# Optimization experiments

Measured on AMD Instinct MI355X. Metric: run time of the kernel, lower is better.

Reference implementation:

```python
import jax, jax.numpy as jnp
import numpy as np

NEG = -1e10
LN_EPS = 1e-5


def _layernorm(x, g, b):
    m = x.mean(-1, keepdims=True)
    v = ((x - m) ** 2).mean(-1, keepdims=True)
    return (x - m) / jnp.sqrt(v + LN_EPS) * g + b


def setup_inputs() -> dict:
    key = jax.random.key(0)
    ks = jax.random.split(key, 12)
    B, N, C, H, E = 8, 2048, 64, 2, 65536
    p = lambda i, shape: (jax.random.normal(ks[i], shape, jnp.float32) * 0.02)
    return {
        "x": jax.random.normal(ks[0], (B, N, C), jnp.float32),
        "edge": jax.random.randint(ks[1], (2, E), 0, N),
        "num_heads": H,
        "wq_d": p(2, (C, C)), "wk_d": p(3, (C, C)), "wv_d": p(4, (C, C)), "bv_d": jnp.zeros((C,), jnp.float32),
        "wq_s": p(5, (C, C)), "wk_s": p(6, (C, C)), "wv_s": p(7, (C, C)), "bv_s": jnp.zeros((C,), jnp.float32),
        "ln1_g": jnp.ones((C,), jnp.float32), "ln1_b": jnp.zeros((C,), jnp.float32),
        "ln2_g": jnp.ones((C,), jnp.float32), "ln2_b": jnp.zeros((C,), jnp.float32),
        "w1": p(8, (C, 2 * C)), "b1": jnp.zeros((2 * C,), jnp.float32),
        "w2": p(9, (2 * C, C)), "b2": jnp.zeros((C,), jnp.float32),
    }


def reference(x, edge, num_heads,
              wq_d, wk_d, wv_d, bv_d,
              wq_s, wk_s, wv_s, bv_s,
              ln1_g, ln1_b, ln2_g, ln2_b,
              w1, b1, w2, b2):
    B, N, C = x.shape
    H = num_heads
    d = C // H
    scale = C ** (-0.5)  # original scales by x.shape[-1]**-0.5, not head dim

    # ---- DMHSA: dynamic mean-threshold masked attention ----
    q = (x @ wq_d).reshape(B, N, H, d).transpose(0, 2, 1, 3)  # [B,H,N,d]
    k = (x @ wk_d).reshape(B, N, H, d).transpose(0, 2, 1, 3)
    v = (x @ wv_d + bv_d).reshape(B, N, H, d).transpose(0, 2, 1, 3)
    scores = jnp.einsum('bhnd,bhmd->bhnm', q, k) * scale  # [B,H,N,N]
    dyn_mask = scores >= scores.mean(-1, keepdims=True)
    attn_d = jax.nn.softmax(jnp.where(dyn_mask, scores, NEG), axis=-1)
    dyn_out = jnp.einsum('bhnm,bhmd->bnhd', attn_d, v).reshape(B, N, C)

    # ---- SSA: static graph-edge masked attention (single head) ----
    qs = x @ wq_s
    ks_ = x @ wk_s
    vs = x @ wv_s + bv_s
    scores_s = jnp.einsum('bnc,bmc->bnm', qs, ks_) * scale  # [B,N,N]
    edge_mask = jnp.zeros((N, N), bool).at[edge[0], edge[1]].set(True)
    attn_s = jax.nn.softmax(jnp.where(edge_mask[None], scores_s, NEG), axis=-1)
    static_out = jnp.einsum('bnm,bmc->bnc', attn_s, vs)

    # ---- residual + LN + MLP (two linears, no activation) + LN ----
    residual = dyn_out + static_out + x
    h = _layernorm(residual, ln1_g, ln1_b)
    h = (h @ w1 + b1) @ w2 + b2
    out = _layernorm(h + residual, ln2_g, ln2_b)
    return (out, attn_d)
```

## Files before the change

### kernel.cpp

```cpp
#include <hip/hip_runtime.h>
#include <hip/hip_bf16.h>

#define TB 256

constexpr int B_ = 8, N_ = 2048, H_ = 2;
constexpr float SCALE = 0.125f;
constexpr float NEGV = -1e10f;
constexpr float LN_EPS = 1e-5f;
constexpr size_t SCH = (size_t)B_ * N_ * 64;

typedef __attribute__((ext_vector_type(8))) short bf16x8;
typedef __attribute__((ext_vector_type(4))) float f32x4;
typedef __attribute__((ext_vector_type(8))) unsigned short us8;
typedef __attribute__((ext_vector_type(4))) unsigned short us4;

#define MFMA16(A, B, C) __builtin_amdgcn_mfma_f32_16x16x32_bf16((A), (B), (C), 0, 0, 0)

__device__ __forceinline__ unsigned short f2b(float f) {
  __hip_bfloat16 h = __float2bfloat16(f);
  return *reinterpret_cast<unsigned short*>(&h);
}
__device__ __forceinline__ float b2f(unsigned short u) {
  union { unsigned int i; float f; } v; v.i = ((unsigned int)u) << 16; return v.f;
}
__device__ __forceinline__ int swz(int off) { return off ^ (((off >> 12) & 7) << 4); }

__device__ __forceinline__ float wave_reduce_sum(float v) {
#pragma unroll
  for (int off = 32; off >= 1; off >>= 1) v += __shfl_xor(v, off, 64);
  return v;
}
__device__ __forceinline__ float wave_reduce_max(float v) {
#pragma unroll
  for (int off = 32; off >= 1; off >>= 1) v = fmaxf(v, __shfl_xor(v, off, 64));
  return v;
}

__global__ __launch_bounds__(TB) void proj_kernel(
    const float* __restrict__ x,
    const float* __restrict__ wqd, const float* __restrict__ wkd,
    const float* __restrict__ wvd, const float* __restrict__ bvd,
    const float* __restrict__ wqs, const float* __restrict__ wks,
    const float* __restrict__ wvs, const float* __restrict__ bvs,
    float* __restrict__ vd, float* __restrict__ vsb,
    unsigned short* __restrict__ q16d, unsigned short* __restrict__ k16d,
    unsigned short* __restrict__ q16s, unsigned short* __restrict__ k16s) {
  const int t = threadIdx.x;
  const int row = blockIdx.x * 16 + (t >> 4);
  const int cg = t & 15;
  const int b = row >> 11, n = row & 2047;
  float xr[64];
  const float4* xp = reinterpret_cast<const float4*>(x + (size_t)row * 64);
#pragma unroll
  for (int i = 0; i < 16; ++i) {
    float4 v = xp[i];
    xr[4 * i] = v.x; xr[4 * i + 1] = v.y; xr[4 * i + 2] = v.z; xr[4 * i + 3] = v.w;
  }
  const float* W[6] = {wqd, wkd, wvd, wqs, wks, wvs};
#pragma unroll
  for (int m = 0; m < 6; ++m) {
    float4 acc = make_float4(0.f, 0.f, 0.f, 0.f);
    if (m == 2) acc = reinterpret_cast<const float4*>(bvd)[cg];
    if (m == 5) acc = reinterpret_cast<const float4*>(bvs)[cg];
    const float4* wp = reinterpret_cast<const float4*>(W[m]) + cg;
#pragma unroll
    for (int c = 0; c < 64; ++c) {
      float4 w4 = wp[(size_t)c * 16];
      float s = xr[c];
      acc.x += s * w4.x; acc.y += s * w4.y; acc.z += s * w4.z; acc.w += s * w4.w;
    }
    if (m == 2) {
      reinterpret_cast<float4*>(vd + (size_t)row * 64)[cg] = acc;
    } else if (m == 5) {
      reinterpret_cast<float4*>(vsb + (size_t)row * 64)[cg] = acc;
    } else {
      float sc = (m == 0 || m == 3) ? SCALE : 1.f;
      us4 o; o.x = f2b(acc.x * sc); o.y = f2b(acc.y * sc);
      o.z = f2b(acc.z * sc); o.w = f2b(acc.w * sc);
      if (m == 0 || m == 1) {
        unsigned short* dst = (m == 0) ? q16d : k16d;
        size_t idx = ((size_t)(b * 2 + (cg >> 3)) * 2048 + n) * 32 + (cg & 7) * 4;
        *reinterpret_cast<us4*>(dst + idx) = o;
      } else {
        unsigned short* dst = (m == 3) ? q16s : k16s;
        *reinterpret_cast<us4*>(dst + (size_t)row * 64 + cg * 4) = o;
      }
    }
  }
}

__global__ __launch_bounds__(TB) void tr32_kernel(const float* __restrict__ v,
                                                  unsigned short* __restrict__ vt) {
  __shared__ float tile[256][33];
  const int t = threadIdx.x;
  const int bh = blockIdx.y, b = bh >> 1, h = bh & 1;
  const int r0 = blockIdx.x * 256;
  const float* src = v + ((size_t)b * 2048 + r0) * 64 + h * 32;
#pragma unroll
  for (int i = 0; i < 8; ++i) {
    int f4 = t + i * 256;
    int row = f4 >> 3, c4 = f4 & 7;
    float4 xv = *reinterpret_cast<const float4*>(src + (size_t)row * 64 + c4 * 4);
    tile[row][c4 * 4 + 0] = xv.x; tile[row][c4 * 4 + 1] = xv.y;
    tile[row][c4 * 4 + 2] = xv.z; tile[row][c4 * 4 + 3] = xv.w;
  }
  __syncthreads();
  unsigned short* dstb = vt + (size_t)bh * 32 * 2048 + r0;
#pragma unroll
  for (int i = 0; i < 4; ++i) {
    int ch = t + i * 256;
    int d = ch >> 5, rb = ch & 31;
    us8 o;
#pragma unroll
    for (int e = 0; e < 8; ++e) o[e] = f2b(tile[rb * 8 + e][d]);
    *reinterpret_cast<us8*>(dstb + (size_t)d * 2048 + rb * 8) = o;
  }
}

__global__ __launch_bounds__(TB) void tr64_kernel(const float* __restrict__ v,
                                                  unsigned short* __restrict__ vt) {
  __shared__ float tile[128][65];
  const int t = threadIdx.x;
  const int b = blockIdx.y;
  const int r0 = blockIdx.x * 128;
  const float* src = v + ((size_t)b * 2048 + r0) * 64;
#pragma unroll
  for (int i = 0; i < 8; ++i) {
    int f4 = t + i * 256;
    int row = f4 >> 4, c4 = f4 & 15;
    float4 xv = *reinterpret_cast<const float4*>(src + (size_t)row * 64 + c4 * 4);
    tile[row][c4 * 4 + 0] = xv.x; tile[row][c4 * 4 + 1] = xv.y;
    tile[row][c4 * 4 + 2] = xv.z; tile[row][c4 * 4 + 3] = xv.w;
  }
  __syncthreads();
  unsigned short* dstb = vt + (size_t)b * 64 * 2048 + r0;
#pragma unroll
  for (int i = 0; i < 4; ++i) {
    int ch = t + i * 256;
    int d = ch >> 4, rb = ch & 15;
    us8 o;
#pragma unroll
    for (int e = 0; e < 8; ++e) o[e] = f2b(tile[rb * 8 + e][d]);
    *reinterpret_cast<us8*>(dstb + (size_t)d * 2048 + rb * 8) = o;
  }
}

__global__ void zero_mask_kernel(unsigned int* __restrict__ mb) {
  mb[(size_t)blockIdx.x * TB + threadIdx.x] = 0u;
}
__global__ void scatter_kernel(const int* __restrict__ edge, int E,
                               unsigned int* __restrict__ mb) {
  int e = blockIdx.x * TB + threadIdx.x;
  if (e < E) {
    int r = edge[e];
    int c = edge[E + e];
    atomicOr(&mb[r * (N_ / 32) + (c >> 5)], 1u << (c & 31));
  }
}

__global__ __launch_bounds__(TB, 2) void dmhsa_kernel(
    const unsigned short* __restrict__ q16, const unsigned short* __restrict__ k16,
    const unsigned short* __restrict__ vt16,
    float* __restrict__ od, float* __restrict__ attn_out) {
  __shared__ __align__(16) char lds[16 * 4096];
  __shared__ float redsum[4][16], redmax[4][16];
  __shared__ float rowmean[16], rowmax[16], rowrinv[16];

  const int t = threadIdx.x, w = t >> 6, lane = t & 63;
  const int g = lane >> 4, m = lane & 15;
  const int bh = blockIdx.y;
  const int row0 = blockIdx.x * 16;
  const size_t qkbase = (size_t)bh * 2048 * 32;

  bf16x8 aq = *reinterpret_cast<const bf16x8*>(q16 + qkbase + (size_t)(row0 + m) * 32 + 8 * g);

  float rs[4] = {0.f, 0.f, 0.f, 0.f};
  float rm[4] = {-1e30f, -1e30f, -1e30f, -1e30f};
  const int c0w = w * 512;
  for (int jt = 0; jt < 32; ++jt) {
    int c0 = c0w + jt * 16;
    bf16x8 bk = *reinterpret_cast<const bf16x8*>(k16 + qkbase + (size_t)(c0 + m) * 32 + 8 * g);
    f32x4 z = {0.f, 0.f, 0.f, 0.f};
    f32x4 acc = MFMA16(aq, bk, z);
#pragma unroll
    for (int r = 0; r < 4; ++r) {
      float v = acc[r];
      rs[r] += v; rm[r] = fmaxf(rm[r], v);
      int row = 4 * g + r;
      *reinterpret_cast<unsigned short*>(lds + swz(row * 4096 + (c0 + m) * 2)) = f2b(v);
    }
  }
#pragma unroll
  for (int off = 1; off < 16; off <<= 1) {
#pragma unroll
    for (int r = 0; r < 4; ++r) {
      rs[r] += __shfl_xor(rs[r], off, 64);
      rm[r] = fmaxf(rm[r], __shfl_xor(rm[r], off, 64));
    }
  }
  if (m == 0) {
#pragma unroll
    for (int r = 0; r < 4; ++r) { redsum[w][4 * g + r] = rs[r]; redmax[w][4 * g + r] = rm[r]; }
  }
  __syncthreads();
  if (t < 16) {
    float s = redsum[0][t] + redsum[1][t] + redsum[2][t] + redsum[3][t];
    float mx = fmaxf(fmaxf(redmax[0][t], redmax[1][t]), fmaxf(redmax[2][t], redmax[3][t]));
    rowmean[t] = s * (1.f / 2048.f);
    rowmax[t] = mx;
  }
  __syncthreads();

#pragma unroll
  for (int rr = 0; rr < 4; ++rr) {
    int row = w * 4 + rr;
    float mean = rowmean[row], mx = rowmax[row];
    float part = 0.f;
#pragma unroll
    for (int kc = 0; kc < 4; ++kc) {
      us8* p = reinterpret_cast<us8*>(lds + swz(row * 4096 + lane * 16 + kc * 1024));
      us8 sv = *p;
      us8 pv;
#pragma unroll
      for (int e = 0; e < 8; ++e) {
        float s = b2f(sv[e]);
        float ev = (s >= mean) ? __expf(s - mx) : 0.f;
        part += ev;
        pv[e] = f2b(ev);
      }
      *p = pv;
    }
    part = wave_reduce_sum(part);
    if (lane == 0) rowrinv[row] = 1.f / part;
  }
  __syncthreads();

  {
    float* aout = attn_out + ((size_t)bh * 2048 + row0) * 2048;
#pragma unroll
    for (int rr = 0; rr < 4; ++rr) {
      int row = w * 4 + rr;
      float rinv = rowrinv[row];
#pragma unroll
      for (int kc = 0; kc < 4; ++kc) {
        us8 pv = *reinterpret_cast<const us8*>(lds + swz(row * 4096 + lane * 16 + kc * 1024));
        int col = lane * 8 + kc * 512;
        float4 o0, o1;
        o0.x = b2f(pv[0]) * rinv; o0.y = b2f(pv[1]) * rinv;
        o0.z = b2f(pv[2]) * rinv; o0.w = b2f(pv[3]) * rinv;
        o1.x = b2f(pv[4]) * rinv; o1.y = b2f(pv[5]) * rinv;
        o1.z = b2f(pv[6]) * rinv; o1.w = b2f(pv[7]) * rinv;
        *reinterpret_cast<float4*>(aout + (size_t)row * 2048 + col) = o0;
        *reinterpret_cast<float4*>(aout + (size_t)row * 2048 + col + 4) = o1;
      }
    }
  }

  f32x4 oa0 = {0.f, 0.f, 0.f, 0.f}, oa1 = {0.f, 0.f, 0.f, 0.f};
  const unsigned short* vtb = vt16 + (size_t)bh * 32 * 2048;
  for (int jc = 0; jc < 16; ++jc) {
    int j0 = w * 512 + jc * 32;
    bf16x8 ap = *reinterpret_cast<const bf16x8*>(lds + swz(m * 4096 + (j0 + 8 * g) * 2));
    bf16x8 bv0 = *reinterpret_cast<const bf16x8*>(vtb + (size_t)m * 2048 + j0 + 8 * g);
    bf16x8 bv1 = *reinterpret_cast<const bf16x8*>(vtb + (size_t)(16 + m) * 2048 + j0 + 8 * g);
    oa0 = MFMA16(ap, bv0, oa0);
    oa1 = MFMA16(ap, bv1, oa1);
  }
  __syncthreads();
  float* obuf = reinterpret_cast<float*>(lds);
#pragma unroll
  for (int r = 0; r < 4; ++r) {
    obuf[(w * 16 + 4 * g + r) * 32 + m] = oa0[r];
    obuf[(w * 16 + 4 * g + r) * 32 + 16 + m] = oa1[r];
  }
  __syncthreads();
  {
    const int b = bh >> 1, h = bh & 1;
    int idx = t;
#pragma unroll
    for (int u = 0; u < 2; ++u, idx += 256) {
      int row = idx >> 5, d = idx & 31;
      float o = obuf[(0 * 16 + row) * 32 + d] + obuf[(1 * 16 + row) * 32 + d] +
                obuf[(2 * 16 + row) * 32 + d] + obuf[(3 * 16 + row) * 32 + d];
      od[((size_t)b * 2048 + row0 + row) * 64 + h * 32 + d] = o * rowrinv[row];
    }
  }
}

__global__ __launch_bounds__(TB, 2) void ssa_kernel(
    const unsigned short* __restrict__ q16, const unsigned short* __restrict__ k16,
    const unsigned short* __restrict__ vt16, const unsigned int* __restrict__ mb,
    float* __restrict__ osb) {
  __shared__ __align__(16) char lds[16 * 4096];
  __shared__ float rowrinv[16];

  const int t = threadIdx.x, w = t >> 6, lane = t & 63;
  const int g = lane >> 4, m = lane & 15;
  const int b = blockIdx.y;
  const int row0 = blockIdx.x * 16;
  const size_t base = (size_t)b * 2048 * 64;

  bf16x8 aq0 = *reinterpret_cast<const bf16x8*>(q16 + base + (size_t)(row0 + m) * 64 + 8 * g);
  bf16x8 aq1 = *reinterpret_cast<const bf16x8*>(q16 + base + (size_t)(row0 + m) * 64 + 32 + 8 * g);

  const int c0w = w * 512;
  for (int jt = 0; jt < 32; ++jt) {
    int c0 = c0w + jt * 16;
    bf16x8 bk0 = *reinterpret_cast<const bf16x8*>(k16 + base + (size_t)(c0 + m) * 64 + 8 * g);
    bf16x8 bk1 = *reinterpret_cast<const bf16x8*>(k16 + base + (size_t)(c0 + m) * 64 + 32 + 8 * g);
    f32x4 z = {0.f, 0.f, 0.f, 0.f};
    f32x4 acc = MFMA16(aq0, bk0, z);
    acc = MFMA16(aq1, bk1, acc);
#pragma unroll
    for (int r = 0; r < 4; ++r) {
      int row = 4 * g + r;
      *reinterpret_cast<unsigned short*>(lds + swz(row * 4096 + (c0 + m) * 2)) = f2b(acc[r]);
    }
  }
  __syncthreads();

#pragma unroll
  for (int rr = 0; rr < 4; ++rr) {
    int row = w * 4 + rr;
    const unsigned char* mbb = reinterpret_cast<const unsigned char*>(mb) + (size_t)(row0 + row) * 256;
    float rmx = -1e30f;
#pragma unroll
    for (int kc = 0; kc < 4; ++kc) {
      us8 sv = *reinterpret_cast<const us8*>(lds + swz(row * 4096 + lane * 16 + kc * 1024));
      unsigned int mby = mbb[lane + kc * 64];
#pragma unroll
      for (int e = 0; e < 8; ++e) {
        float s = ((mby >> e) & 1u) ? b2f(sv[e]) : NEGV;
        rmx = fmaxf(rmx, s);
      }
    }
    rmx = wave_reduce_max(rmx);
    float part = 0.f;
#pragma unroll
    for (int kc = 0; kc < 4; ++kc) {
      us8* p = reinterpret_cast<us8*>(lds + swz(row * 4096 + lane * 16 + kc * 1024));
      us8 sv = *p;
      us8 pv;
#pragma unroll
      for (int e = 0; e < 8; ++e) {
        float s = ((mbb[lane + kc * 64] >> e) & 1u) ? b2f(sv[e]) : NEGV;
        float ev = __expf(s - rmx);
        part += ev;
        pv[e] = f2b(ev);
      }
      *p = pv;
    }
    part = wave_reduce_sum(part);
    if (lane == 0) rowrinv[row] = 1.f / part;
  }
  __syncthreads();

  f32x4 oa[4];
#pragma unroll
  for (int d = 0; d < 4; ++d) oa[d] = (f32x4){0.f, 0.f, 0.f, 0.f};
  const unsigned short* vtb = vt16 + (size_t)b * 64 * 2048;
  for (int jc = 0; jc < 16; ++jc) {
    int j0 = w * 512 + jc * 32;
    bf16x8 ap = *reinterpret_cast<const bf16x8*>(lds + swz(m * 4096 + (j0 + 8 * g) * 2));
#pragma unroll
    for (int db = 0; db < 4; ++db) {
      bf16x8 bv = *reinterpret_cast<const bf16x8*>(vtb + (size_t)(db * 16 + m) * 2048 + j0 + 8 * g);
      oa[db] = MFMA16(ap, bv, oa[db]);
    }
  }
  __syncthreads();
  float* obuf = reinterpret_cast<float*>(lds);
#pragma unroll
  for (int db = 0; db < 4; ++db)
#pragma unroll
    for (int r = 0; r < 4; ++r)
      obuf[(w * 16 + 4 * g + r) * 64 + db * 16 + m] = oa[db][r];
  __syncthreads();
  {
    int idx = t;
#pragma unroll
    for (int u = 0; u < 4; ++u, idx += 256) {
      int row = idx >> 6, d = idx & 63;
      float o = obuf[(0 * 16 + row) * 64 + d] + obuf[(1 * 16 + row) * 64 + d] +
                obuf[(2 * 16 + row) * 64 + d] + obuf[(3 * 16 + row) * 64 + d];
      osb[base + (size_t)(row0 + row) * 64 + d] = o * rowrinv[row];
    }
  }
}

__global__ __launch_bounds__(TB) void epi_kernel(
    const float* __restrict__ x, const float* __restrict__ od,
    const float* __restrict__ osb,
    const float* __restrict__ g1, const float* __restrict__ bb1,
    const float* __restrict__ g2, const float* __restrict__ bb2,
    const float* __restrict__ w1, const float* __restrict__ bm1,
    const float* __restrict__ w2, const float* __restrict__ bm2,
    float* __restrict__ out) {
  __shared__ float hl[4][64];
  __shared__ float tl[4][128];
  const int t = threadIdx.x, wv = t >> 6, c = t & 63;
  const size_t row = (size_t)blockIdx.x * 4 + wv;
  const size_t base = row * 64 + c;
  float res = od[base] + osb[base] + x[base];
  float mean = wave_reduce_sum(res) * (1.f / 64.f);
  float dlt = res - mean;
  float var = wave_reduce_sum(dlt * dlt) * (1.f / 64.f);
  float hval = dlt * rsqrtf(var + LN_EPS) * g1[c] + bb1[c];
  hl[wv][c] = hval;
  __syncthreads();
  float t0 = bm1[2 * c], t1 = bm1[2 * c + 1];
#pragma unroll 16
  for (int cc = 0; cc < 64; ++cc) {
    float hv = hl[wv][cc];
    float2 wv2 = *reinterpret_cast<const float2*>(w1 + (size_t)cc * 128 + 2 * c);
    t0 += hv * wv2.x; t1 += hv * wv2.y;
  }
  *reinterpret_cast<float2*>(&tl[wv][2 * c]) = make_float2(t0, t1);
  __syncthreads();
  float mo = bm2[c];
#pragma unroll 8
  for (int j4 = 0; j4 < 32; ++j4) {
    float4 t4 = *reinterpret_cast<const float4*>(&tl[wv][j4 * 4]);
    mo += t4.x * w2[(size_t)(j4 * 4 + 0) * 64 + c];
    mo += t4.y * w2[(size_t)(j4 * 4 + 1) * 64 + c];
    mo += t4.z * w2[(size_t)(j4 * 4 + 2) * 64 + c];
    mo += t4.w * w2[(size_t)(j4 * 4 + 3) * 64 + c];
  }
  float y = mo + res;
  float mean2 = wave_reduce_sum(y) * (1.f / 64.f);
  float d2 = y - mean2;
  float var2 = wave_reduce_sum(d2 * d2) * (1.f / 64.f);
  out[base] = d2 * rsqrtf(var2 + LN_EPS) * g2[c] + bb2[c];
}

extern "C" void kernel_launch(void* const* d_in, const int* in_sizes, int n_in,
                              void* d_out, int out_size, void* d_ws, size_t ws_size,
                              hipStream_t stream) {
  const float* x    = (const float*)d_in[0];
  const int*   edge = (const int*)d_in[1];
  const float* wqd = (const float*)d_in[3];
  const float* wkd = (const float*)d_in[4];
  const float* wvd = (const float*)d_in[5];
  const float* bvd = (const float*)d_in[6];
  const float* wqs = (const float*)d_in[7];
  const float* wks = (const float*)d_in[8];
  const float* wvs = (const float*)d_in[9];
  const float* bvs = (const float*)d_in[10];
  const float* g1  = (const float*)d_in[11];
  const float* b1g = (const float*)d_in[12];
  const float* g2  = (const float*)d_in[13];
  const float* b2g = (const float*)d_in[14];
  const float* w1  = (const float*)d_in[15];
  const float* bm1 = (const float*)d_in[16];
  const float* w2  = (const float*)d_in[17];
  const float* bm2 = (const float*)d_in[18];
  const int E = in_sizes[1] / 2;

  float* out  = (float*)d_out;
  float* attn = out + SCH;

  char* W = (char*)d_ws;
  float*          vd    = (float*)(W);
  float*          vsb   = (float*)(W + ((size_t)4  << 20));
  float*          od    = (float*)(W + ((size_t)8  << 20));
  float*          osb   = (float*)(W + ((size_t)12 << 20));
  unsigned short* q16d  = (unsigned short*)(W + ((size_t)16 << 20));
  unsigned short* k16d  = (unsigned short*)(W + ((size_t)18 << 20));
  unsigned short* q16s  = (unsigned short*)(W + ((size_t)20 << 20));
  unsigned short* k16s  = (unsigned short*)(W + ((size_t)22 << 20));
  unsigned short* vt16d = (unsigned short*)(W + ((size_t)24 << 20));
  unsigned short* vt16s = (unsigned short*)(W + ((size_t)26 << 20));
  unsigned int*   mb    = (unsigned int*)(W + ((size_t)28 << 20));

  proj_kernel<<<(B_ * N_) / 16, TB, 0, stream>>>(x, wqd, wkd, wvd, bvd, wqs, wks, wvs, bvs,
                                                 vd, vsb, q16d, k16d, q16s, k16s);
  tr32_kernel<<<dim3(8, 16), TB, 0, stream>>>(vd, vt16d);
  tr64_kernel<<<dim3(16, 8), TB, 0, stream>>>(vsb, vt16s);
  zero_mask_kernel<<<(N_ * N_ / 32) / TB, TB, 0, stream>>>(mb);
  scatter_kernel<<<(E + TB - 1) / TB, TB, 0, stream>>>(edge, E, mb);
  dmhsa_kernel<<<dim3(128, 16), TB, 0, stream>>>(q16d, k16d, vt16d, od, attn);
  ssa_kernel<<<dim3(128, 8), TB, 0, stream>>>(q16s, k16s, vt16s, mb, osb);
  epi_kernel<<<(B_ * N_) / 4, TB, 0, stream>>>(x, od, osb, g1, b1g, g2, b2g, w1, bm1, w2, bm2, out);
}
```

Baseline: 558.4 us.

## Use 512-thread blocks for attention kernels, splitting columns over eight waves

Doubles the thread count of the dynamic and static attention kernels from 256 to 512. Each of eight waves now covers 256 score columns and two softmax rows instead of 512 columns and four rows, and the cross-wave reductions grow to eight partials. The aim is more latency hiding and more parallel work per 64KB LDS tile, since LDS use per block stays the same. It also hoists the mask byte load out of the inner element loop in the SSA kernel, at the cost of more sync participants and larger reduction loops.

```diff
diff --git a/kernel.cpp b/kernel.cpp
--- a/kernel.cpp
+++ b/kernel.cpp
@@ -2,6 +2,7 @@
 #include <hip/hip_bf16.h>
 
 #define TB 256
+#define TBA 512
 
 constexpr int B_ = 8, N_ = 2048, H_ = 2;
 constexpr float SCALE = 0.125f;
@@ -158,12 +159,12 @@
   }
 }
 
-__global__ __launch_bounds__(TB, 2) void dmhsa_kernel(
+__global__ __launch_bounds__(TBA, 4) void dmhsa_kernel(
     const unsigned short* __restrict__ q16, const unsigned short* __restrict__ k16,
     const unsigned short* __restrict__ vt16,
     float* __restrict__ od, float* __restrict__ attn_out) {
   __shared__ __align__(16) char lds[16 * 4096];
-  __shared__ float redsum[4][16], redmax[4][16];
+  __shared__ float redsum[8][16], redmax[8][16];
   __shared__ float rowmean[16], rowmax[16], rowrinv[16];
 
   const int t = threadIdx.x, w = t >> 6, lane = t & 63;
@@ -176,8 +177,8 @@
 
   float rs[4] = {0.f, 0.f, 0.f, 0.f};
   float rm[4] = {-1e30f, -1e30f, -1e30f, -1e30f};
-  const int c0w = w * 512;
-  for (int jt = 0; jt < 32; ++jt) {
+  const int c0w = w * 256;
+  for (int jt = 0; jt < 16; ++jt) {
     int c0 = c0w + jt * 16;
     bf16x8 bk = *reinterpret_cast<const bf16x8*>(k16 + qkbase + (size_t)(c0 + m) * 32 + 8 * g);
     f32x4 z = {0.f, 0.f, 0.f, 0.f};
@@ -204,16 +205,20 @@
   }
   __syncthreads();
   if (t < 16) {
-    float s = redsum[0][t] + redsum[1][t] + redsum[2][t] + redsum[3][t];
-    float mx = fmaxf(fmaxf(redmax[0][t], redmax[1][t]), fmaxf(redmax[2][t], redmax[3][t]));
+    float s = 0.f, mx = -1e30f;
+#pragma unroll
+    for (int ww = 0; ww < 8; ++ww) {
+      s += redsum[ww][t];
+      mx = fmaxf(mx, redmax[ww][t]);
+    }
     rowmean[t] = s * (1.f / 2048.f);
     rowmax[t] = mx;
   }
   __syncthreads();
 
 #pragma unroll
-  for (int rr = 0; rr < 4; ++rr) {
-    int row = w * 4 + rr;
+  for (int rr = 0; rr < 2; ++rr) {
+    int row = w * 2 + rr;
     float mean = rowmean[row], mx = rowmax[row];
     float part = 0.f;
 #pragma unroll
@@ -238,8 +243,8 @@
   {
     float* aout = attn_out + ((size_t)bh * 2048 + row0) * 2048;
 #pragma unroll
-    for (int rr = 0; rr < 4; ++rr) {
-      int row = w * 4 + rr;
+    for (int rr = 0; rr < 2; ++rr) {
+      int row = w * 2 + rr;
       float rinv = rowrinv[row];
 #pragma unroll
       for (int kc = 0; kc < 4; ++kc) {
@@ -258,8 +263,8 @@
 
   f32x4 oa0 = {0.f, 0.f, 0.f, 0.f}, oa1 = {0.f, 0.f, 0.f, 0.f};
   const unsigned short* vtb = vt16 + (size_t)bh * 32 * 2048;
-  for (int jc = 0; jc < 16; ++jc) {
-    int j0 = w * 512 + jc * 32;
+  for (int jc = 0; jc < 8; ++jc) {
+    int j0 = w * 256 + jc * 32;
     bf16x8 ap = *reinterpret_cast<const bf16x8*>(lds + swz(m * 4096 + (j0 + 8 * g) * 2));
     bf16x8 bv0 = *reinterpret_cast<const bf16x8*>(vtb + (size_t)m * 2048 + j0 + 8 * g);
     bf16x8 bv1 = *reinterpret_cast<const bf16x8*>(vtb + (size_t)(16 + m) * 2048 + j0 + 8 * g);
@@ -276,18 +281,15 @@
   __syncthreads();
   {
     const int b = bh >> 1, h = bh & 1;
-    int idx = t;
-#pragma unroll
-    for (int u = 0; u < 2; ++u, idx += 256) {
-      int row = idx >> 5, d = idx & 31;
-      float o = obuf[(0 * 16 + row) * 32 + d] + obuf[(1 * 16 + row) * 32 + d] +
-                obuf[(2 * 16 + row) * 32 + d] + obuf[(3 * 16 + row) * 32 + d];
-      od[((size_t)b * 2048 + row0 + row) * 64 + h * 32 + d] = o * rowrinv[row];
-    }
-  }
-}
-
-__global__ __launch_bounds__(TB, 2) void ssa_kernel(
+    int row = t >> 5, d = t & 31;
+    float o = 0.f;
+#pragma unroll
+    for (int s = 0; s < 8; ++s) o += obuf[(s * 16 + row) * 32 + d];
+    od[((size_t)b * 2048 + row0 + row) * 64 + h * 32 + d] = o * rowrinv[row];
+  }
+}
+
+__global__ __launch_bounds__(TBA, 4) void ssa_kernel(
     const unsigned short* __restrict__ q16, const unsigned short* __restrict__ k16,
     const unsigned short* __restrict__ vt16, const unsigned int* __restrict__ mb,
     float* __restrict__ osb) {
@@ -303,8 +305,8 @@
   bf16x8 aq0 = *reinterpret_cast<const bf16x8*>(q16 + base + (size_t)(row0 + m) * 64 + 8 * g);
   bf16x8 aq1 = *reinterpret_cast<const bf16x8*>(q16 + base + (size_t)(row0 + m) * 64 + 32 + 8 * g);
 
-  const int c0w = w * 512;
-  for (int jt = 0; jt < 32; ++jt) {
+  const int c0w = w * 256;
+  for (int jt = 0; jt < 16; ++jt) {
     int c0 = c0w + jt * 16;
     bf16x8 bk0 = *reinterpret_cast<const bf16x8*>(k16 + base + (size_t)(c0 + m) * 64 + 8 * g);
     bf16x8 bk1 = *reinterpret_cast<const bf16x8*>(k16 + base + (size_t)(c0 + m) * 64 + 32 + 8 * g);
@@ -320,8 +322,8 @@
   __syncthreads();
 
 #pragma unroll
-  for (int rr = 0; rr < 4; ++rr) {
-    int row = w * 4 + rr;
+  for (int rr = 0; rr < 2; ++rr) {
+    int row = w * 2 + rr;
     const unsigned char* mbb = reinterpret_cast<const unsigned char*>(mb) + (size_t)(row0 + row) * 256;
     float rmx = -1e30f;
 #pragma unroll
@@ -341,9 +343,10 @@
       us8* p = reinterpret_cast<us8*>(lds + swz(row * 4096 + lane * 16 + kc * 1024));
       us8 sv = *p;
       us8 pv;
+      unsigned int mby = mbb[lane + kc * 64];
 #pragma unroll
       for (int e = 0; e < 8; ++e) {
-        float s = ((mbb[lane + kc * 64] >> e) & 1u) ? b2f(sv[e]) : NEGV;
+        float s = ((mby >> e) & 1u) ? b2f(sv[e]) : NEGV;
         float ev = __expf(s - rmx);
         part += ev;
         pv[e] = f2b(ev);
@@ -359,8 +362,8 @@
 #pragma unroll
   for (int d = 0; d < 4; ++d) oa[d] = (f32x4){0.f, 0.f, 0.f, 0.f};
   const unsigned short* vtb = vt16 + (size_t)b * 64 * 2048;
-  for (int jc = 0; jc < 16; ++jc) {
-    int j0 = w * 512 + jc * 32;
+  for (int jc = 0; jc < 8; ++jc) {
+    int j0 = w * 256 + jc * 32;
     bf16x8 ap = *reinterpret_cast<const bf16x8*>(lds + swz(m * 4096 + (j0 + 8 * g) * 2));
 #pragma unroll
     for (int db = 0; db < 4; ++db) {
@@ -377,12 +380,13 @@
       obuf[(w * 16 + 4 * g + r) * 64 + db * 16 + m] = oa[db][r];
   __syncthreads();
   {
-    int idx = t;
-#pragma unroll
-    for (int u = 0; u < 4; ++u, idx += 256) {
+#pragma unroll
+    for (int u = 0; u < 2; ++u) {
+      int idx = t + u * TBA;
       int row = idx >> 6, d = idx & 63;
-      float o = obuf[(0 * 16 + row) * 64 + d] + obuf[(1 * 16 + row) * 64 + d] +
-                obuf[(2 * 16 + row) * 64 + d] + obuf[(3 * 16 + row) * 64 + d];
+      float o = 0.f;
+#pragma unroll
+      for (int s = 0; s < 8; ++s) o += obuf[(s * 16 + row) * 64 + d];
       osb[base + (size_t)(row0 + row) * 64 + d] = o * rowrinv[row];
     }
   }
@@ -478,7 +482,7 @@
   tr64_kernel<<<dim3(16, 8), TB, 0, stream>>>(vsb, vt16s);
   zero_mask_kernel<<<(N_ * N_ / 32) / TB, TB, 0, stream>>>(mb);
   scatter_kernel<<<(E + TB - 1) / TB, TB, 0, stream>>>(edge, E, mb);
-  dmhsa_kernel<<<dim3(128, 16), TB, 0, stream>>>(q16d, k16d, vt16d, od, attn);
-  ssa_kernel<<<dim3(128, 8), TB, 0, stream>>>(q16s, k16s, vt16s, mb, osb);
+  dmhsa_kernel<<<dim3(128, 16), TBA, 0, stream>>>(q16d, k16d, vt16d, od, attn);
+  ssa_kernel<<<dim3(128, 8), TBA, 0, stream>>>(q16s, k16s, vt16s, mb, osb);
   epi_kernel<<<(B_ * N_) / 4, TB, 0, stream>>>(x, od, osb, g1, b1g, g2, b2g, w1, bm1, w2, bm2, out);
 }
```

New measurement: 540.9 us. -3.1%, faster.
